# Performance work log

Measured on AMD Instinct MI355X. Metric: run time of the kernel, lower is better.

Reference implementation:

```python
import jax, jax.numpy as jnp
import numpy as np

B, T, D, M = 8, 4096, 64, 1024  # batch, frames, embedding_dim, codebook size


def setup_inputs() -> dict:
    key = jax.random.key(0)
    k1, k2, k3 = jax.random.split(key, 3)
    x = jax.random.normal(k1, (B, D, T), dtype=jnp.float32)          # (B, channels=D, T)
    embedding = jax.random.normal(k2, (M, D), dtype=jnp.float32)     # codebook
    # Precomputed Gumbel noise, matching torch: -log(-log(clamp(U, eps, 1-eps)))
    eps = jnp.finfo(jnp.float32).eps
    u = jax.random.uniform(k3, (B * T, M), dtype=jnp.float32)
    gumbels = -jnp.log(-jnp.log(jnp.clip(u, eps, 1.0 - eps)))
    log_var_q = jnp.float32(0.0)
    temperature = jnp.float32(0.5)
    return {"x": x, "embedding": embedding, "log_var_q": log_var_q,
            "gumbels": gumbels, "temperature": temperature}


def reference(x, embedding, log_var_q, gumbels, temperature):
    B_, D_, T_ = x.shape
    M_ = embedding.shape[0]
    xt = jnp.swapaxes(x, 1, 2)                 # (B, T, D)
    x_flat = xt.reshape(-1, D_)                # (N, D)
    precision = jnp.exp(-log_var_q)            # scalar
    # 0.5 * precision * ||x - e||^2, via the GEMM expansion (fused cdist)
    sq = (jnp.sum(x_flat * x_flat, axis=1, keepdims=True)
          + jnp.sum(embedding * embedding, axis=1)[None, :]
          - 2.0 * x_flat @ embedding.T)        # (N, M)
    distances = 0.5 * precision * sq
    indices = jnp.argmin(distances, axis=-1)   # (N,)
    logits = -distances
    # gumbel-softmax (soft)
    encodings = jax.nn.softmax((logits + gumbels) / temperature, axis=-1)  # (N, M)
    quantized = (encodings @ embedding).reshape(B_, T_, D_)                # (B, T, D)
    logits3 = logits.reshape(B_, T_, M_)
    log_probs = jax.nn.log_softmax(logits3, axis=-1)
    probs = jnp.exp(log_probs)
    recon = 0.5 * precision * jnp.sum((xt - quantized) ** 2, axis=(1, 2))  # (B,)
    neg_entropy = jnp.sum(probs * log_probs, axis=(1, 2))                  # (B,)
    loss = jnp.mean(recon + neg_entropy)
    # perplexity over hard assignments
    one_hot = jax.nn.one_hot(indices, M_, dtype=jnp.float32)               # (N, M)
    avg_probs = jnp.mean(one_hot, axis=0)
    perplexity = jnp.exp(-jnp.sum(avg_probs * jnp.log(avg_probs + 1e-10)))
    return jnp.swapaxes(quantized, 1, 2), loss, perplexity
```

## Files before the change

### kernel.cpp

```cpp
#include <hip/hip_runtime.h>

#define T_DIM 4096
#define D_DIM 64
#define M_DIM 1024
#define N_ROWS 32768
#define TR 16
#define NT 256

typedef __attribute__((ext_vector_type(8))) short bf16x8;
typedef __attribute__((ext_vector_type(4))) float f32x4;

#define WS_BF16_OFF 4096

__device__ __forceinline__ short f2bfs(float f) {
  union { float f; unsigned u; } v; v.f = f;
  unsigned r = v.u + 0x7fffu + ((v.u >> 16) & 1u);
  return (short)(r >> 16);
}
__device__ __forceinline__ float bf2f(short h) {
  union { unsigned u; float f; } v; v.u = ((unsigned)(unsigned short)h) << 16;
  return v.f;
}
__device__ __forceinline__ void cvt8(const float* p, bf16x8& h8, bf16x8& l8) {
  float4 a = *(const float4*)p, b = *(const float4*)(p + 4);
  float v[8] = {a.x, a.y, a.z, a.w, b.x, b.y, b.z, b.w};
#pragma unroll
  for (int i = 0; i < 8; ++i) {
    short h = f2bfs(v[i]);
    h8[i] = h;
    l8[i] = f2bfs(v[i] - bf2f(h));
  }
}

__global__ void vq_conv(const float* __restrict__ emb, float* __restrict__ ws) {
  __shared__ short s_h[64][72], s_l[64][72];
  const int tid = threadIdx.x;
  const int mb = blockIdx.x * 64;
  short* EH = (short*)(ws + WS_BF16_OFF);
  short* EL = EH + 65536;
  short* ETH = EL + 65536;
  short* ETL = ETH + 65536;
#pragma unroll
  for (int i = 0; i < 16; ++i) {
    int lin = tid + 256 * i;
    int ml = lin >> 6, d = lin & 63;
    float v = emb[(size_t)(mb + ml) * 64 + d];
    short h = f2bfs(v);
    short l = f2bfs(v - bf2f(h));
    EH[(size_t)(mb + ml) * 64 + d] = h;
    EL[(size_t)(mb + ml) * 64 + d] = l;
    s_h[d][ml] = h;
    s_l[d][ml] = l;
  }
  if (tid < 64) {
    const float* e = emb + (size_t)(mb + tid) * 64;
    float s = 0.f;
#pragma unroll
    for (int d = 0; d < 64; d += 4) {
      float4 v = *(const float4*)(e + d);
      s += v.x * v.x + v.y * v.y + v.z * v.z + v.w * v.w;
    }
    ws[mb + tid] = s;
    ws[M_DIM + mb + tid] = 0.f;
  }
  if (blockIdx.x == 0 && tid == 0) ws[2 * M_DIM] = 0.f;
  __syncthreads();
#pragma unroll
  for (int i = 0; i < 16; ++i) {
    int lin = tid + 256 * i;
    int d = lin >> 6, ml = lin & 63;
    ETH[(size_t)d * 1024 + mb + ml] = s_h[d][ml];
    ETL[(size_t)d * 1024 + mb + ml] = s_l[d][ml];
  }
}

__global__ __launch_bounds__(NT, 4) void vq_main(
    const float* __restrict__ x, const float* __restrict__ emb,
    const float* __restrict__ lvq, const float* __restrict__ gum,
    const float* __restrict__ temp, float* __restrict__ outq,
    float* __restrict__ ws) {
  __shared__ float s_x[TR][68];
  __shared__ float s_xx[TR];
  __shared__ float s_qp[4][TR][68];
  __shared__ float s_stA_m[4][TR];
  __shared__ int   s_stA_i[4][TR];
  __shared__ float s_stB[4][TR][3];
  __shared__ float s_stC[4][TR];
  __shared__ float s_red[4];

  const int tid = threadIdx.x;
  const int lane = tid & 63;
  const int wl = tid >> 6;
  const int mq = lane >> 4;
  const int mn = lane & 15;
  const int n0 = blockIdx.x * TR;
  const int b = n0 >> 12;
  const int t0 = n0 & (T_DIM - 1);
  const float precision = __expf(-lvq[0]);
  const float inv_temp = 1.0f / temp[0];
  const float* eew = ws;
  float* counts = ws + M_DIM;
  float* accum = ws + 2 * M_DIM;
  const short* EH = (const short*)(ws + WS_BF16_OFF);
  const short* EL = EH + 65536;
  const short* ETH = EL + 65536;
  const short* ETL = ETH + 65536;

  {
    int tt = tid & 15, d0 = tid >> 4;
#pragma unroll
    for (int k = 0; k < 4; ++k) {
      int d = d0 + 16 * k;
      s_x[tt][d] = x[((size_t)b << 18) + ((size_t)d << 12) + (size_t)(t0 + tt)];
    }
  }
  __syncthreads();
  if (tid < TR) {
    float s = 0.f;
#pragma unroll
    for (int d = 0; d < D_DIM; ++d) { float v = s_x[tid][d]; s += v * v; }
    s_xx[tid] = s;
  }
  __syncthreads();

  f32x4 acc[16];
  {
    bf16x8 ah0, al0, ah1, al1;
    cvt8(&s_x[mn][mq * 8], ah0, al0);
    cvt8(&s_x[mn][32 + mq * 8], ah1, al1);
#pragma unroll
    for (int tt = 0; tt < 16; ++tt) acc[tt] = (f32x4){0.f, 0.f, 0.f, 0.f};
#pragma unroll
    for (int tt = 0; tt < 16; ++tt) {
      int m0 = wl * 256 + tt * 16;
      const short* bp = EH + (m0 + mn) * 64 + mq * 8;
      const short* lp = EL + (m0 + mn) * 64 + mq * 8;
      bf16x8 bh0 = *(const bf16x8*)bp;
      bf16x8 bh1 = *(const bf16x8*)(bp + 32);
      bf16x8 bl0 = *(const bf16x8*)lp;
      bf16x8 bl1 = *(const bf16x8*)(lp + 32);
      acc[tt] = __builtin_amdgcn_mfma_f32_16x16x32_bf16(ah0, bh0, acc[tt], 0, 0, 0);
      acc[tt] = __builtin_amdgcn_mfma_f32_16x16x32_bf16(ah1, bh1, acc[tt], 0, 0, 0);
      acc[tt] = __builtin_amdgcn_mfma_f32_16x16x32_bf16(al0, bh0, acc[tt], 0, 0, 0);
      acc[tt] = __builtin_amdgcn_mfma_f32_16x16x32_bf16(al1, bh1, acc[tt], 0, 0, 0);
      acc[tt] = __builtin_amdgcn_mfma_f32_16x16x32_bf16(ah0, bl0, acc[tt], 0, 0, 0);
      acc[tt] = __builtin_amdgcn_mfma_f32_16x16x32_bf16(ah1, bl1, acc[tt], 0, 0, 0);
    }
    float xx4[4];
#pragma unroll
    for (int reg = 0; reg < 4; ++reg) xx4[reg] = s_xx[mq * 4 + reg];
#pragma unroll
    for (int tt = 0; tt < 16; ++tt) {
      float eev = eew[wl * 256 + tt * 16 + mn];
#pragma unroll
      for (int reg = 0; reg < 4; ++reg)
        acc[tt][reg] = precision * (acc[tt][reg] - 0.5f * (xx4[reg] + eev));
    }
  }

  float Mx[4]; int Mi[4];
#pragma unroll
  for (int reg = 0; reg < 4; ++reg) {
    float mx = acc[0][reg]; int mi = wl * 256 + mn;
#pragma unroll
    for (int tt = 1; tt < 16; ++tt) {
      float v = acc[tt][reg];
      int m = wl * 256 + tt * 16 + mn;
      if (v > mx) { mx = v; mi = m; }
    }
#pragma unroll
    for (int off = 1; off <= 8; off <<= 1) {
      float omx = __shfl_xor(mx, off);
      int omi = __shfl_xor(mi, off);
      if (omx > mx || (omx == mx && omi < mi)) { mx = omx; mi = omi; }
    }
    if (mn == 0) { s_stA_m[wl][mq * 4 + reg] = mx; s_stA_i[wl][mq * 4 + reg] = mi; }
  }
  __syncthreads();
#pragma unroll
  for (int reg = 0; reg < 4; ++reg) {
    int token = mq * 4 + reg;
    Mx[reg] = s_stA_m[0][token]; Mi[reg] = s_stA_i[0][token];
#pragma unroll
    for (int w = 1; w < 4; ++w) {
      float m2 = s_stA_m[w][token]; int i2 = s_stA_i[w][token];
      if (m2 > Mx[reg] || (m2 == Mx[reg] && i2 < Mi[reg])) { Mx[reg] = m2; Mi[reg] = i2; }
    }
  }
  float partial = 0.f;
  if (wl == 0 && mn == 0) {
#pragma unroll
    for (int reg = 0; reg < 4; ++reg) atomicAdd(counts + Mi[reg], 1.0f);
  }

  float Zs[4] = {0.f, 0.f, 0.f, 0.f}, As[4] = {0.f, 0.f, 0.f, 0.f}, Gm[4];
#pragma unroll
  for (int reg = 0; reg < 4; ++reg) {
    const float* gp = gum + ((size_t)(n0 + mq * 4 + reg) << 10) + wl * 256 + mn;
    float gm = -1e30f;
#pragma unroll
    for (int tt = 0; tt < 16; ++tt) {
      float g = gp[tt * 16];
      float s = acc[tt][reg];
      float a = s - Mx[reg];
      float e = __expf(a);
      Zs[reg] += e; As[reg] += a * e;
      float gv = (s + g) * inv_temp;
      acc[tt][reg] = gv;
      gm = fmaxf(gm, gv);
    }
    Gm[reg] = gm;
  }
#pragma unroll
  for (int reg = 0; reg < 4; ++reg) {
#pragma unroll
    for (int off = 1; off <= 8; off <<= 1) {
      Zs[reg] += __shfl_xor(Zs[reg], off);
      As[reg] += __shfl_xor(As[reg], off);
      Gm[reg] = fmaxf(Gm[reg], __shfl_xor(Gm[reg], off));
    }
    if (mn == 0) {
      s_stB[wl][mq * 4 + reg][0] = Zs[reg];
      s_stB[wl][mq * 4 + reg][1] = As[reg];
      s_stB[wl][mq * 4 + reg][2] = Gm[reg];
    }
  }
  __syncthreads();
  float GM[4];
#pragma unroll
  for (int reg = 0; reg < 4; ++reg) {
    int token = mq * 4 + reg;
    float zs = 0.f, as = 0.f, gmax = -1e30f;
#pragma unroll
    for (int w = 0; w < 4; ++w) {
      zs += s_stB[w][token][0];
      as += s_stB[w][token][1];
      gmax = fmaxf(gmax, s_stB[w][token][2]);
    }
    GM[reg] = gmax;
    if (wl == 0 && mn == 0) partial += as / zs - __logf(zs);
  }
  float Zg[4] = {0.f, 0.f, 0.f, 0.f};
#pragma unroll
  for (int tt = 0; tt < 16; ++tt) {
#pragma unroll
    for (int reg = 0; reg < 4; ++reg) {
      float p = __expf(acc[tt][reg] - GM[reg]);
      acc[tt][reg] = p;
      Zg[reg] += p;
    }
  }
#pragma unroll
  for (int reg = 0; reg < 4; ++reg) {
#pragma unroll
    for (int off = 1; off <= 8; off <<= 1) Zg[reg] += __shfl_xor(Zg[reg], off);
    if (mn == 0) s_stC[wl][mq * 4 + reg] = Zg[reg];
  }
  __syncthreads();
  float invZg[4];
#pragma unroll
  for (int reg = 0; reg < 4; ++reg) {
    int token = mq * 4 + reg;
    float z = 0.f;
#pragma unroll
    for (int w = 0; w < 4; ++w) z += s_stC[w][token];
    invZg[reg] = 1.0f / z;
  }

  {
    f32x4 q[4];
#pragma unroll
    for (int nt = 0; nt < 4; ++nt) q[nt] = (f32x4){0.f, 0.f, 0.f, 0.f};
    float* sp = &s_qp[wl][0][0];
#pragma unroll
    for (int ks = 0; ks < 8; ++ks) {
#pragma unroll
      for (int reg = 0; reg < 4; ++reg) {
        sp[(mq * 4 + reg) * 36 + mn]      = acc[2 * ks][reg] * invZg[reg];
        sp[(mq * 4 + reg) * 36 + 16 + mn] = acc[2 * ks + 1][reg] * invZg[reg];
      }
      bf16x8 ph, pl;
      cvt8(&sp[mn * 36 + mq * 8], ph, pl);
      int k0 = wl * 256 + ks * 32;
#pragma unroll
      for (int nt = 0; nt < 4; ++nt) {
        const short* bp = ETH + (nt * 16 + mn) * 1024 + k0 + mq * 8;
        const short* lp = ETL + (nt * 16 + mn) * 1024 + k0 + mq * 8;
        bf16x8 bh = *(const bf16x8*)bp;
        bf16x8 bl = *(const bf16x8*)lp;
        q[nt] = __builtin_amdgcn_mfma_f32_16x16x32_bf16(ph, bh, q[nt], 0, 0, 0);
        q[nt] = __builtin_amdgcn_mfma_f32_16x16x32_bf16(pl, bh, q[nt], 0, 0, 0);
        q[nt] = __builtin_amdgcn_mfma_f32_16x16x32_bf16(ph, bl, q[nt], 0, 0, 0);
      }
    }
#pragma unroll
    for (int nt = 0; nt < 4; ++nt)
#pragma unroll
      for (int reg = 0; reg < 4; ++reg)
        s_qp[wl][mq * 4 + reg][nt * 16 + mn] = q[nt][reg];
  }
  __syncthreads();

  {
    int r = tid & 15, dq = tid >> 4;
    float4 qs = {0.f, 0.f, 0.f, 0.f};
#pragma unroll
    for (int w = 0; w < 4; ++w) {
      float4 v = *(const float4*)&s_qp[w][r][4 * dq];
      qs.x += v.x; qs.y += v.y; qs.z += v.z; qs.w += v.w;
    }
    int t = t0 + r;
    float* ob = outq + ((size_t)b << 18) + (size_t)t;
    int d = 4 * dq;
    ob[(size_t)(d + 0) << 12] = qs.x;
    ob[(size_t)(d + 1) << 12] = qs.y;
    ob[(size_t)(d + 2) << 12] = qs.z;
    ob[(size_t)(d + 3) << 12] = qs.w;
    float4 xv = *(const float4*)&s_x[r][d];
    float dx0 = xv.x - qs.x, dx1 = xv.y - qs.y, dx2 = xv.z - qs.z, dx3 = xv.w - qs.w;
    partial += 0.5f * precision * (dx0 * dx0 + dx1 * dx1 + dx2 * dx2 + dx3 * dx3);
  }
#pragma unroll
  for (int off = 32; off; off >>= 1) partial += __shfl_xor(partial, off);
  if (lane == 0) s_red[wl] = partial;
  __syncthreads();
  if (tid == 0)
    atomicAdd(accum, s_red[0] + s_red[1] + s_red[2] + s_red[3]);
}

__global__ void vq_finalize(const float* __restrict__ ws, float* __restrict__ out) {
  __shared__ float red[4];
  int tid = threadIdx.x;
  float h = 0.f;
  for (int m = tid; m < M_DIM; m += 256) {
    float avg = ws[M_DIM + m] * (1.0f / 32768.0f);
    h += avg * __logf(avg + 1e-10f);
  }
#pragma unroll
  for (int off = 32; off; off >>= 1) h += __shfl_xor(h, off);
  int lane = tid & 63, wave = tid >> 6;
  if (lane == 0) red[wave] = h;
  __syncthreads();
  if (tid == 0) {
    out[0] = ws[2 * M_DIM] * 0.125f;
    out[1] = __expf(-(red[0] + red[1] + red[2] + red[3]));
  }
}

extern "C" void kernel_launch(void* const* d_in, const int* in_sizes, int n_in,
                              void* d_out, int out_size, void* d_ws, size_t ws_size,
                              hipStream_t stream) {
  const float* x = (const float*)d_in[0];
  const float* emb = (const float*)d_in[1];
  const float* lvq = (const float*)d_in[2];
  const float* gum = (const float*)d_in[3];
  const float* temp = (const float*)d_in[4];
  float* out = (float*)d_out;
  float* ws = (float*)d_ws;

  hipLaunchKernelGGL(vq_conv, dim3(16), dim3(256), 0, stream, emb, ws);
  hipLaunchKernelGGL(vq_main, dim3(N_ROWS / TR), dim3(NT), 0, stream,
                     x, emb, lvq, gum, temp, out, ws);
  hipLaunchKernelGGL(vq_finalize, dim3(1), dim3(256), 0, stream, ws,
                     out + (size_t)2097152);
}
```

Baseline: 335.2 us.

## Split codebook across eight waves per block instead of four

Doubles the block size to 512 threads so each wave handles 128 codebook entries instead of 256. This halves the per-wave accumulator registers and the per-wave MFMA, Gumbel-load and softmax work. The aim is more waves in flight to hide the latency of the Gumbel-noise and codebook loads. In exchange the cross-wave reductions through shared memory double in width, shared memory per block grows, and launch_bounds(512,4) may squeeze VGPRs enough to cause spills.

```diff
diff --git a/kernel.cpp b/kernel.cpp
--- a/kernel.cpp
+++ b/kernel.cpp
@@ -5,7 +5,8 @@
 #define M_DIM 1024
 #define N_ROWS 32768
 #define TR 16
-#define NT 256
+#define NT 512
+#define NW 8
 
 typedef __attribute__((ext_vector_type(8))) short bf16x8;
 typedef __attribute__((ext_vector_type(4))) float f32x4;
@@ -81,12 +82,12 @@
     float* __restrict__ ws) {
   __shared__ float s_x[TR][68];
   __shared__ float s_xx[TR];
-  __shared__ float s_qp[4][TR][68];
-  __shared__ float s_stA_m[4][TR];
-  __shared__ int   s_stA_i[4][TR];
-  __shared__ float s_stB[4][TR][3];
-  __shared__ float s_stC[4][TR];
-  __shared__ float s_red[4];
+  __shared__ float s_qp[NW][TR][68];
+  __shared__ float s_stA_m[NW][TR];
+  __shared__ int   s_stA_i[NW][TR];
+  __shared__ float s_stB[NW][TR][3];
+  __shared__ float s_stC[NW][TR];
+  __shared__ float s_red[NW];
 
   const int tid = threadIdx.x;
   const int lane = tid & 63;
@@ -108,11 +109,9 @@
 
   {
     int tt = tid & 15, d0 = tid >> 4;
-#pragma unroll
-    for (int k = 0; k < 4; ++k) {
-      int d = d0 + 16 * k;
-      s_x[tt][d] = x[((size_t)b << 18) + ((size_t)d << 12) + (size_t)(t0 + tt)];
-    }
+    s_x[tt][d0] = x[((size_t)b << 18) + ((size_t)d0 << 12) + (size_t)(t0 + tt)];
+    s_x[tt][d0 + 32] =
+        x[((size_t)b << 18) + ((size_t)(d0 + 32) << 12) + (size_t)(t0 + tt)];
   }
   __syncthreads();
   if (tid < TR) {
@@ -123,16 +122,16 @@
   }
   __syncthreads();
 
-  f32x4 acc[16];
+  f32x4 acc[8];
   {
     bf16x8 ah0, al0, ah1, al1;
     cvt8(&s_x[mn][mq * 8], ah0, al0);
     cvt8(&s_x[mn][32 + mq * 8], ah1, al1);
 #pragma unroll
-    for (int tt = 0; tt < 16; ++tt) acc[tt] = (f32x4){0.f, 0.f, 0.f, 0.f};
-#pragma unroll
-    for (int tt = 0; tt < 16; ++tt) {
-      int m0 = wl * 256 + tt * 16;
+    for (int tt = 0; tt < 8; ++tt) acc[tt] = (f32x4){0.f, 0.f, 0.f, 0.f};
+#pragma unroll
+    for (int tt = 0; tt < 8; ++tt) {
+      int m0 = wl * 128 + tt * 16;
       const short* bp = EH + (m0 + mn) * 64 + mq * 8;
       const short* lp = EL + (m0 + mn) * 64 + mq * 8;
       bf16x8 bh0 = *(const bf16x8*)bp;
@@ -150,8 +149,8 @@
 #pragma unroll
     for (int reg = 0; reg < 4; ++reg) xx4[reg] = s_xx[mq * 4 + reg];
 #pragma unroll
-    for (int tt = 0; tt < 16; ++tt) {
-      float eev = eew[wl * 256 + tt * 16 + mn];
+    for (int tt = 0; tt < 8; ++tt) {
+      float eev = eew[wl * 128 + tt * 16 + mn];
 #pragma unroll
       for (int reg = 0; reg < 4; ++reg)
         acc[tt][reg] = precision * (acc[tt][reg] - 0.5f * (xx4[reg] + eev));
@@ -161,11 +160,11 @@
   float Mx[4]; int Mi[4];
 #pragma unroll
   for (int reg = 0; reg < 4; ++reg) {
-    float mx = acc[0][reg]; int mi = wl * 256 + mn;
-#pragma unroll
-    for (int tt = 1; tt < 16; ++tt) {
+    float mx = acc[0][reg]; int mi = wl * 128 + mn;
+#pragma unroll
+    for (int tt = 1; tt < 8; ++tt) {
       float v = acc[tt][reg];
-      int m = wl * 256 + tt * 16 + mn;
+      int m = wl * 128 + tt * 16 + mn;
       if (v > mx) { mx = v; mi = m; }
     }
 #pragma unroll
@@ -182,7 +181,7 @@
     int token = mq * 4 + reg;
     Mx[reg] = s_stA_m[0][token]; Mi[reg] = s_stA_i[0][token];
 #pragma unroll
-    for (int w = 1; w < 4; ++w) {
+    for (int w = 1; w < NW; ++w) {
       float m2 = s_stA_m[w][token]; int i2 = s_stA_i[w][token];
       if (m2 > Mx[reg] || (m2 == Mx[reg] && i2 < Mi[reg])) { Mx[reg] = m2; Mi[reg] = i2; }
     }
@@ -196,10 +195,10 @@
   float Zs[4] = {0.f, 0.f, 0.f, 0.f}, As[4] = {0.f, 0.f, 0.f, 0.f}, Gm[4];
 #pragma unroll
   for (int reg = 0; reg < 4; ++reg) {
-    const float* gp = gum + ((size_t)(n0 + mq * 4 + reg) << 10) + wl * 256 + mn;
+    const float* gp = gum + ((size_t)(n0 + mq * 4 + reg) << 10) + wl * 128 + mn;
     float gm = -1e30f;
 #pragma unroll
-    for (int tt = 0; tt < 16; ++tt) {
+    for (int tt = 0; tt < 8; ++tt) {
       float g = gp[tt * 16];
       float s = acc[tt][reg];
       float a = s - Mx[reg];
@@ -232,7 +231,7 @@
     int token = mq * 4 + reg;
     float zs = 0.f, as = 0.f, gmax = -1e30f;
 #pragma unroll
-    for (int w = 0; w < 4; ++w) {
+    for (int w = 0; w < NW; ++w) {
       zs += s_stB[w][token][0];
       as += s_stB[w][token][1];
       gmax = fmaxf(gmax, s_stB[w][token][2]);
@@ -242,7 +241,7 @@
   }
   float Zg[4] = {0.f, 0.f, 0.f, 0.f};
 #pragma unroll
-  for (int tt = 0; tt < 16; ++tt) {
+  for (int tt = 0; tt < 8; ++tt) {
 #pragma unroll
     for (int reg = 0; reg < 4; ++reg) {
       float p = __expf(acc[tt][reg] - GM[reg]);
@@ -263,7 +262,7 @@
     int token = mq * 4 + reg;
     float z = 0.f;
 #pragma unroll
-    for (int w = 0; w < 4; ++w) z += s_stC[w][token];
+    for (int w = 0; w < NW; ++w) z += s_stC[w][token];
     invZg[reg] = 1.0f / z;
   }
 
@@ -273,7 +272,7 @@
     for (int nt = 0; nt < 4; ++nt) q[nt] = (f32x4){0.f, 0.f, 0.f, 0.f};
     float* sp = &s_qp[wl][0][0];
 #pragma unroll
-    for (int ks = 0; ks < 8; ++ks) {
+    for (int ks = 0; ks < 4; ++ks) {
 #pragma unroll
       for (int reg = 0; reg < 4; ++reg) {
         sp[(mq * 4 + reg) * 36 + mn]      = acc[2 * ks][reg] * invZg[reg];
@@ -281,7 +280,7 @@
       }
       bf16x8 ph, pl;
       cvt8(&sp[mn * 36 + mq * 8], ph, pl);
-      int k0 = wl * 256 + ks * 32;
+      int k0 = wl * 128 + ks * 32;
 #pragma unroll
       for (int nt = 0; nt < 4; ++nt) {
         const short* bp = ETH + (nt * 16 + mn) * 1024 + k0 + mq * 8;
@@ -301,11 +300,11 @@
   }
   __syncthreads();
 
-  {
+  if (tid < 256) {
     int r = tid & 15, dq = tid >> 4;
     float4 qs = {0.f, 0.f, 0.f, 0.f};
 #pragma unroll
-    for (int w = 0; w < 4; ++w) {
+    for (int w = 0; w < NW; ++w) {
       float4 v = *(const float4*)&s_qp[w][r][4 * dq];
       qs.x += v.x; qs.y += v.y; qs.z += v.z; qs.w += v.w;
     }
@@ -324,8 +323,12 @@
   for (int off = 32; off; off >>= 1) partial += __shfl_xor(partial, off);
   if (lane == 0) s_red[wl] = partial;
   __syncthreads();
-  if (tid == 0)
-    atomicAdd(accum, s_red[0] + s_red[1] + s_red[2] + s_red[3]);
+  if (tid == 0) {
+    float s = 0.f;
+#pragma unroll
+    for (int w = 0; w < NW; ++w) s += s_red[w];
+    atomicAdd(accum, s);
+  }
 }
 
 __global__ void vq_finalize(const float* __restrict__ ws, float* __restrict__ out) {
```

Result: faster. 316.8 us (-5.5%).
